# Optimization experiments

Hardware: AMD Instinct MI355X
Metric: run time of the kernel (lower is better)

Reference implementation:

```python
import jax, jax.numpy as jnp
import numpy as np
from jax.ops import segment_sum

NEG_SLOPE = 0.01  # torch F.leaky_relu default

N_NODES = 100000
N_EDGES = 1600000
IN_FEAT = 67
HIDDEN = 256
N_CLASS = 18
N_GRAPHS = 256


def setup_inputs() -> dict:
    key = jax.random.key(0)
    ks = jax.random.split(key, 12)
    h = jax.random.normal(ks[0], (N_NODES, IN_FEAT), dtype=jnp.float32)
    src = jax.random.randint(ks[1], (N_EDGES,), 0, N_NODES, dtype=jnp.int32)
    dst = jax.random.randint(ks[2], (N_EDGES,), 0, N_NODES, dtype=jnp.int32)
    graph_ids = jnp.sort(jax.random.randint(ks[3], (N_NODES,), 0, N_GRAPHS, dtype=jnp.int32))
    s = 0.05
    W1_self = jax.random.normal(ks[4], (IN_FEAT, HIDDEN), dtype=jnp.float32) * s
    W1_neigh = jax.random.normal(ks[5], (IN_FEAT, HIDDEN), dtype=jnp.float32) * s
    b1 = jnp.zeros((HIDDEN,), dtype=jnp.float32)
    W2_self = jax.random.normal(ks[6], (HIDDEN, HIDDEN), dtype=jnp.float32) * s
    W2_neigh = jax.random.normal(ks[7], (HIDDEN, HIDDEN), dtype=jnp.float32) * s
    b2 = jnp.zeros((HIDDEN,), dtype=jnp.float32)
    Wfc = jax.random.normal(ks[8], (HIDDEN, N_CLASS), dtype=jnp.float32) * s
    bfc = jnp.zeros((N_CLASS,), dtype=jnp.float32)
    return {
        "h": h, "W1_self": W1_self, "W1_neigh": W1_neigh, "b1": b1,
        "W2_self": W2_self, "W2_neigh": W2_neigh, "b2": b2,
        "Wfc": Wfc, "bfc": bfc,
        "src": src, "dst": dst, "graph_ids": graph_ids, "num_graphs": N_GRAPHS,
    }


def _sage_mean(h, Wself, Wneigh, b, src, dst, n_nodes):
    # DGL SAGEConv(mean): h_neigh = mean over incoming neighbors; 0 if no neighbors
    agg = segment_sum(h[src], dst, num_segments=n_nodes)          # [N, D]
    deg = segment_sum(jnp.ones_like(dst, dtype=h.dtype), dst, num_segments=n_nodes)
    h_neigh = agg / jnp.maximum(deg, 1.0)[:, None]
    return h @ Wself + h_neigh @ Wneigh + b


def reference(h, W1_self, W1_neigh, b1, W2_self, W2_neigh, b2, Wfc, bfc,
              src, dst, graph_ids, num_graphs):
    n_nodes = h.shape[0]
    x = jax.nn.leaky_relu(_sage_mean(h, W1_self, W1_neigh, b1, src, dst, n_nodes), NEG_SLOPE)
    x = jax.nn.leaky_relu(_sage_mean(x, W2_self, W2_neigh, b2, src, dst, n_nodes), NEG_SLOPE)
    # dgl.mean_nodes: per-graph mean pooling over nodes
    gsum = segment_sum(x, graph_ids, num_segments=num_graphs)       # [G, D]
    gcnt = segment_sum(jnp.ones((n_nodes,), dtype=x.dtype), graph_ids, num_segments=num_graphs)
    hg = gsum / jnp.maximum(gcnt, 1.0)[:, None]
    return hg @ Wfc + bfc  # [G, n_classifier]
```

## Files before the change

kernel.cpp:

```cpp
#include <hip/hip_runtime.h>

#define WAVE 64
#define OW 256
#define LDA1 96

typedef short bf16x8 __attribute__((ext_vector_type(8)));
typedef float f32x4  __attribute__((ext_vector_type(4)));

__device__ __forceinline__ unsigned short f2bf(float f) {
    unsigned int u = __float_as_uint(f);
    u = (u + 0x7FFF + ((u >> 16) & 1)) >> 16;
    return (unsigned short)u;
}
__device__ __forceinline__ float bf2f(unsigned short u) {
    return __uint_as_float(((unsigned int)u) << 16);
}
__device__ __forceinline__ float bflo(unsigned int u) { return __uint_as_float(u << 16); }
__device__ __forceinline__ float bfhi(unsigned int u) { return __uint_as_float(u & 0xFFFF0000u); }
__device__ __forceinline__ unsigned int packbf(float lo, float hi) {
    return (unsigned int)f2bf(lo) | ((unsigned int)f2bf(hi) << 16);
}
__device__ __forceinline__ float lrelu(float x) { return x > 0.0f ? x : 0.01f * x; }


__device__ __forceinline__ void pack_b_body(const float* __restrict__ Ws,
                                            const float* __restrict__ Wn,
                                            unsigned short* __restrict__ Bb,
                                            int KHALF, int KT_HALF, int idx) {
    int e  = idx & 7;
    int l  = (idx >> 3) & 63;
    int nt = (idx >> 9) & 15;
    int kt = idx >> 13;
    int n  = nt * 16 + (l & 15);
    int kh = (kt < KT_HALF ? kt : kt - KT_HALF) * 32 + (l >> 4) * 8 + e;
    const float* W = (kt < KT_HALF) ? Ws : Wn;
    float v = (kh < KHALF) ? W[(size_t)kh * OW + n] : 0.0f;
    Bb[idx] = f2bf(v);
}

__global__ void prep_kernel(const float* __restrict__ h, unsigned int* __restrict__ hb,
                            int N, int K,
                            const float* __restrict__ W1s, const float* __restrict__ W1n,
                            unsigned short* __restrict__ Bb1,
                            const float* __restrict__ W2s, const float* __restrict__ W2n,
                            unsigned short* __restrict__ Bb2,
                            const int* __restrict__ dst, int* __restrict__ cnt,
                            int* __restrict__ rank, int E) {
    const int tid = blockIdx.x * blockDim.x + threadIdx.x;
    const int nth = gridDim.x * blockDim.x;

    const int tot_h = N * (LDA1 / 2);
    for (int i = tid; i < tot_h; i += nth) {
        int row = i / (LDA1 / 2);
        int c   = (i - row * (LDA1 / 2)) * 2;
        float v0 = (c     < K) ? h[(size_t)row * K + c]     : 0.0f;
        float v1 = (c + 1 < K) ? h[(size_t)row * K + c + 1] : 0.0f;
        hb[i] = packbf(v0, v1);
    }
    for (int i = tid; i < 2 * 3 * 16 * 64 * 8; i += nth)
        pack_b_body(W1s, W1n, Bb1, K, 3, i);
    for (int i = tid; i < 2 * 8 * 16 * 64 * 8; i += nth)
        pack_b_body(W2s, W2n, Bb2, OW, 8, i);
    const int e4 = E >> 2;
    const int4* dst4 = (const int4*)dst;
    int4* rank4 = (int4*)rank;
    for (int i = tid; i < e4; i += nth) {
        int4 d = dst4[i];
        int4 r;
        r.x = atomicAdd(&cnt[d.x], 1);
        r.y = atomicAdd(&cnt[d.y], 1);
        r.z = atomicAdd(&cnt[d.z], 1);
        r.w = atomicAdd(&cnt[d.w], 1);
        rank4[i] = r;
    }
    for (int e = e4 * 4 + tid; e < E; e += nth)
        rank[e] = atomicAdd(&cnt[dst[e]], 1);
}


__global__ __launch_bounds__(1024) void scan_blocksum(const int* __restrict__ cnt,
                                                      int* __restrict__ bsum, int n) {
    __shared__ int s[1024];
    int i = blockIdx.x * 1024 + threadIdx.x;
    s[threadIdx.x] = (i < n) ? cnt[i] : 0;
    __syncthreads();
    for (int off = 512; off > 0; off >>= 1) {
        if (threadIdx.x < off) s[threadIdx.x] += s[threadIdx.x + off];
        __syncthreads();
    }
    if (threadIdx.x == 0) bsum[blockIdx.x] = s[0];
}

__global__ __launch_bounds__(128) void scan_offsets(int* __restrict__ bsum, int nb) {
    __shared__ int s[128];
    int v = (threadIdx.x < nb) ? bsum[threadIdx.x] : 0;
    s[threadIdx.x] = v;
    __syncthreads();
    for (int off = 1; off < 128; off <<= 1) {
        int t = (threadIdx.x >= off) ? s[threadIdx.x - off] : 0;
        __syncthreads();
        s[threadIdx.x] += t;
        __syncthreads();
    }
    if (threadIdx.x < nb) bsum[threadIdx.x] = s[threadIdx.x] - v;
}

__global__ __launch_bounds__(1024) void scan_write(const int* __restrict__ cnt,
                                                   const int* __restrict__ boff,
                                                   int* __restrict__ rowptr, int n) {
    __shared__ int s[1024];
    int i = blockIdx.x * 1024 + threadIdx.x;
    int v = (i < n) ? cnt[i] : 0;
    s[threadIdx.x] = v;
    __syncthreads();
    for (int off = 1; off < 1024; off <<= 1) {
        int t = (threadIdx.x >= off) ? s[threadIdx.x - off] : 0;
        __syncthreads();
        s[threadIdx.x] += t;
        __syncthreads();
    }
    if (i < n) rowptr[i + 1] = boff[blockIdx.x] + s[threadIdx.x];
    if (i == 0) rowptr[0] = 0;
}

__global__ void fill_kernel(const int* __restrict__ src, const int* __restrict__ dst,
                            const int* __restrict__ rank, const int* __restrict__ rowptr,
                            int* __restrict__ csr_src, int E) {
    const int tid = blockIdx.x * blockDim.x + threadIdx.x;
    const int nth = gridDim.x * blockDim.x;
    const int e4 = E >> 2;
    const int4* dst4 = (const int4*)dst;
    const int4* src4 = (const int4*)src;
    const int4* rank4 = (const int4*)rank;
    for (int i = tid; i < e4; i += nth) {
        int4 d = dst4[i];
        int4 s = src4[i];
        int4 r = rank4[i];
        csr_src[rowptr[d.x] + r.x] = s.x;
        csr_src[rowptr[d.y] + r.y] = s.y;
        csr_src[rowptr[d.z] + r.z] = s.z;
        csr_src[rowptr[d.w] + r.w] = s.w;
    }
    for (int e = e4 * 4 + tid; e < E; e += nth)
        csr_src[rowptr[dst[e]] + rank[e]] = src[e];
}


__global__ void gather_mean256_half(const unsigned int* __restrict__ feat,
                                    const int* __restrict__ rowptr, const int* __restrict__ csr,
                                    unsigned int* __restrict__ aggm, int N, int colhalf) {
    const int lane = threadIdx.x & (WAVE - 1);
    const int grp  = lane >> 4;
    const int sub  = lane & 15;
    const int cb   = colhalf * 64;
    int wave = (blockIdx.x * blockDim.x + threadIdx.x) / WAVE;
    int nw   = (gridDim.x * blockDim.x) / WAVE;

    for (int v = wave; v < N; v += nw) {
        const int beg = rowptr[v], deg = rowptr[v + 1] - beg;
        float l0 = 0.f, h0 = 0.f, l1 = 0.f, h1 = 0.f,
              l2 = 0.f, h2 = 0.f, l3 = 0.f, h3 = 0.f;

        const int noct = deg >> 3;
        for (int i = 0; i < noct; ++i) {
            int e0 = csr[beg + 8 * i + grp];
            int e1 = csr[beg + 8 * i + 4 + grp];
            uint4 x0 = *(const uint4*)(feat + (size_t)e0 * 128 + cb + sub * 4);
            uint4 x1 = *(const uint4*)(feat + (size_t)e1 * 128 + cb + sub * 4);
            l0 += bflo(x0.x) + bflo(x1.x); h0 += bfhi(x0.x) + bfhi(x1.x);
            l1 += bflo(x0.y) + bflo(x1.y); h1 += bfhi(x0.y) + bfhi(x1.y);
            l2 += bflo(x0.z) + bflo(x1.z); h2 += bfhi(x0.z) + bfhi(x1.z);
            l3 += bflo(x0.w) + bflo(x1.w); h3 += bfhi(x0.w) + bfhi(x1.w);
        }
        for (int e = (noct << 3) + grp; e < deg; e += 4) {
            int s = csr[beg + e];
            uint4 x = *(const uint4*)(feat + (size_t)s * 128 + cb + sub * 4);
            l0 += bflo(x.x); h0 += bfhi(x.x);
            l1 += bflo(x.y); h1 += bfhi(x.y);
            l2 += bflo(x.z); h2 += bfhi(x.z);
            l3 += bflo(x.w); h3 += bfhi(x.w);
        }
        l0 += __shfl_xor(l0, 16); l0 += __shfl_xor(l0, 32);
        h0 += __shfl_xor(h0, 16); h0 += __shfl_xor(h0, 32);
        l1 += __shfl_xor(l1, 16); l1 += __shfl_xor(l1, 32);
        h1 += __shfl_xor(h1, 16); h1 += __shfl_xor(h1, 32);
        l2 += __shfl_xor(l2, 16); l2 += __shfl_xor(l2, 32);
        h2 += __shfl_xor(h2, 16); h2 += __shfl_xor(h2, 32);
        l3 += __shfl_xor(l3, 16); l3 += __shfl_xor(l3, 32);
        h3 += __shfl_xor(h3, 16); h3 += __shfl_xor(h3, 32);

        if (grp == 0) {
            float inv = 1.0f / fmaxf((float)deg, 1.0f);
            uint4 o;
            o.x = packbf(l0 * inv, h0 * inv);
            o.y = packbf(l1 * inv, h1 * inv);
            o.z = packbf(l2 * inv, h2 * inv);
            o.w = packbf(l3 * inv, h3 * inv);
            *(uint4*)(aggm + (size_t)v * 128 + cb + sub * 4) = o;
        }
    }
}

__global__ void gather_mean_pad(const unsigned int* __restrict__ feat,
                                const int* __restrict__ rowptr, const int* __restrict__ csr,
                                unsigned int* __restrict__ aggm, int N) {
    const int lane = threadIdx.x & (WAVE - 1);
    const int half = lane >> 5;
    const int sub  = lane & 31;
    const bool act = sub < 24;
    int wave = (blockIdx.x * blockDim.x + threadIdx.x) / WAVE;
    int nw   = (gridDim.x * blockDim.x) / WAVE;

    for (int v = wave; v < N; v += nw) {
        const int beg = rowptr[v], deg = rowptr[v + 1] - beg;
        const int npairs = deg >> 1;
        float l0 = 0.f, h0 = 0.f, l1 = 0.f, h1 = 0.f;

        int p = 0;
        for (; p + 3 < npairs; p += 4) {
            int i0 = csr[beg + 2 * (p + 0) + half];
            int i1 = csr[beg + 2 * (p + 1) + half];
            int i2 = csr[beg + 2 * (p + 2) + half];
            int i3 = csr[beg + 2 * (p + 3) + half];
            if (act) {
                uint2 x0 = *(const uint2*)(feat + (size_t)i0 * 48 + sub * 2);
                uint2 x1 = *(const uint2*)(feat + (size_t)i1 * 48 + sub * 2);
                uint2 x2 = *(const uint2*)(feat + (size_t)i2 * 48 + sub * 2);
                uint2 x3 = *(const uint2*)(feat + (size_t)i3 * 48 + sub * 2);
                l0 += bflo(x0.x) + bflo(x1.x) + bflo(x2.x) + bflo(x3.x);
                h0 += bfhi(x0.x) + bfhi(x1.x) + bfhi(x2.x) + bfhi(x3.x);
                l1 += bflo(x0.y) + bflo(x1.y) + bflo(x2.y) + bflo(x3.y);
                h1 += bfhi(x0.y) + bfhi(x1.y) + bfhi(x2.y) + bfhi(x3.y);
            }
        }
        for (; p < npairs; ++p) {
            int i0 = csr[beg + 2 * p + half];
            if (act) {
                uint2 x0 = *(const uint2*)(feat + (size_t)i0 * 48 + sub * 2);
                l0 += bflo(x0.x); h0 += bfhi(x0.x);
                l1 += bflo(x0.y); h1 += bfhi(x0.y);
            }
        }
        if ((deg & 1) && half == 0) {
            int i0 = csr[beg + deg - 1];
            if (act) {
                uint2 x0 = *(const uint2*)(feat + (size_t)i0 * 48 + sub * 2);
                l0 += bflo(x0.x); h0 += bfhi(x0.x);
                l1 += bflo(x0.y); h1 += bfhi(x0.y);
            }
        }
        l0 += __shfl_xor(l0, 32); h0 += __shfl_xor(h0, 32);
        l1 += __shfl_xor(l1, 32); h1 += __shfl_xor(h1, 32);

        if (half == 0 && act) {
            float inv = 1.0f / fmaxf((float)deg, 1.0f);
            uint2 o;
            o.x = packbf(l0 * inv, h0 * inv);
            o.y = packbf(l1 * inv, h1 * inv);
            *(uint2*)(aggm + (size_t)v * 48 + sub * 2) = o;
        }
    }
}

template<int KT_HALF, int CHUNK>
__global__ __launch_bounds__(512) void sage_mfma(
    const unsigned short* __restrict__ Hs, const unsigned short* __restrict__ Hn, int lda,
    const unsigned short* __restrict__ Bb, const float* __restrict__ bias,
    unsigned short* __restrict__ outb, int M)
{
    constexpr int NT    = 2 * KT_HALF;
    constexpr int NCH   = NT / CHUNK;
    constexpr int CELEM = CHUNK * 16 * 64;
    constexpr int CPT   = CELEM / 512;
    __shared__ bf16x8 Bs[CELEM];

    const int t    = threadIdx.x;
    const int lane = t & 63, wid = t >> 6;
    const int wm   = wid >> 1, wn = wid & 1;
    const int brow = blockIdx.x * 128;
    const int lrow = lane & 15, kblk = lane >> 4;

    const int r0 = brow + wm * 32 + lrow;
    const int r1 = r0 + 16;
    const int r0c = (r0 < M) ? r0 : (M - 1);
    const int r1c = (r1 < M) ? r1 : (M - 1);

    f32x4 acc[2][8];
#pragma unroll
    for (int rt = 0; rt < 2; ++rt)
#pragma unroll
        for (int ct = 0; ct < 8; ++ct) acc[rt][ct] = (f32x4)0.0f;

    for (int ch = 0; ch < NCH; ++ch) {
        bf16x8 a0[CHUNK], a1[CHUNK];
#pragma unroll
        for (int k = 0; k < CHUNK; ++k) {
            int kt = ch * CHUNK + k;
            bool self = kt < KT_HALF;
            int kh = (self ? kt : kt - KT_HALF) * 32 + kblk * 8;
            const unsigned short* srcp = self ? Hs : Hn;
            a0[k] = *(const bf16x8*)(srcp + (size_t)r0c * lda + kh);
            a1[k] = *(const bf16x8*)(srcp + (size_t)r1c * lda + kh);
        }
        const bf16x8* gB = (const bf16x8*)Bb + (size_t)ch * CELEM;
        bf16x8 tmp[CPT];
#pragma unroll
        for (int i = 0; i < CPT; ++i) tmp[i] = gB[i * 512 + t];
        __syncthreads();
#pragma unroll
        for (int i = 0; i < CPT; ++i) Bs[i * 512 + t] = tmp[i];
        __syncthreads();
#pragma unroll
        for (int k = 0; k < CHUNK; ++k) {
            const bf16x8* bp = &Bs[(k * 16 + wn * 8) * 64 + lane];
#pragma unroll
            for (int ct = 0; ct < 8; ++ct) {
                bf16x8 b = bp[ct * 64];
                acc[0][ct] = __builtin_amdgcn_mfma_f32_16x16x32_bf16(a0[k], b, acc[0][ct], 0, 0, 0);
                acc[1][ct] = __builtin_amdgcn_mfma_f32_16x16x32_bf16(a1[k], b, acc[1][ct], 0, 0, 0);
            }
        }
    }

#pragma unroll
    for (int rt = 0; rt < 2; ++rt) {
        int rbase = brow + wm * 32 + rt * 16 + kblk * 4;
#pragma unroll
        for (int ct = 0; ct < 8; ++ct) {
            int col = wn * 128 + ct * 16 + lrow;
            float vb = bias[col];
#pragma unroll
            for (int j = 0; j < 4; ++j) {
                int row = rbase + j;
                if (row < M)
                    outb[(size_t)row * OW + col] = f2bf(lrelu(acc[rt][ct][j] + vb));
            }
        }
    }
}


__global__ __launch_bounds__(256) void pool_fc_kernel(
    const unsigned short* __restrict__ x, const int* __restrict__ gid,
    const float* __restrict__ Wfc, const float* __restrict__ bfc,
    float* __restrict__ out, int N, int C)
{
    int g = blockIdx.x;
    int lo = 0, hi = N;
    while (lo < hi) { int m = (lo + hi) >> 1; if (gid[m] < g) lo = m + 1; else hi = m; }
    int beg = lo;
    hi = N;
    while (lo < hi) { int m = (lo + hi) >> 1; if (gid[m] <= g) lo = m + 1; else hi = m; }
    int end = lo;

    __shared__ float hg[OW];
    int c = threadIdx.x;
    float s0 = 0.f, s1 = 0.f, s2 = 0.f, s3 = 0.f;
    int r = beg;
    for (; r + 3 < end; r += 4) {
        s0 += bf2f(x[(size_t)(r + 0) * OW + c]);
        s1 += bf2f(x[(size_t)(r + 1) * OW + c]);
        s2 += bf2f(x[(size_t)(r + 2) * OW + c]);
        s3 += bf2f(x[(size_t)(r + 3) * OW + c]);
    }
    for (; r < end; ++r) s0 += bf2f(x[(size_t)r * OW + c]);
    float s = (s0 + s1) + (s2 + s3);
    float inv = (end > beg) ? 1.0f / (float)(end - beg) : 0.0f;
    hg[c] = s * inv;
    __syncthreads();

    if (c < C) {
        float a = bfc[c];
        for (int k = 0; k < OW; ++k)
            a = fmaf(hg[k], Wfc[(size_t)k * C + c], a);
        out[(size_t)g * C + c] = a;
    }
}

extern "C" void kernel_launch(void* const* d_in, const int* in_sizes, int n_in,
                              void* d_out, int out_size, void* d_ws, size_t ws_size,
                              hipStream_t stream) {
    const float* h   = (const float*)d_in[0];
    const float* W1s = (const float*)d_in[1];
    const float* W1n = (const float*)d_in[2];
    const float* b1  = (const float*)d_in[3];
    const float* W2s = (const float*)d_in[4];
    const float* W2n = (const float*)d_in[5];
    const float* b2  = (const float*)d_in[6];
    const float* Wfc = (const float*)d_in[7];
    const float* bfc = (const float*)d_in[8];
    const int*   src = (const int*)d_in[9];
    const int*   dst = (const int*)d_in[10];
    const int*   gid = (const int*)d_in[11];

    const int N  = in_sizes[11];
    const int E  = in_sizes[9];
    const int K1 = in_sizes[0] / N;
    const int NC = in_sizes[8];
    const int G  = out_size / NC;

    char* w = (char*)d_ws;
    auto alloc = [&](size_t bytes) { char* p = w; w += (bytes + 255) & ~(size_t)255; return p; };
    unsigned int*   hb     = (unsigned int*)alloc((size_t)N * (LDA1 / 2) * 4);
    unsigned int*   agg1b  = (unsigned int*)alloc((size_t)N * (LDA1 / 2) * 4);
    unsigned short* x1b    = (unsigned short*)alloc((size_t)N * OW * 2);
    unsigned short* agg2b  = (unsigned short*)alloc((size_t)N * OW * 2);
    int*            rowptr = (int*)alloc((size_t)(N + 1) * 4);
    int*            cnt    = (int*)alloc((size_t)N * 4);
    int*            csr    = (int*)alloc((size_t)E * 4);
    int*            rank   = (int*)alloc((size_t)E * 4);
    int*            bsum   = (int*)alloc(1024 * 4);
    unsigned short* Bb1    = (unsigned short*)alloc((size_t)2 * 3 * 16 * 64 * 8 * 2);
    unsigned short* Bb2    = (unsigned short*)alloc((size_t)2 * 8 * 16 * 64 * 8 * 2);

    float* out = (float*)d_out;
    const int nb = (N + 1023) / 1024;

    hipMemsetAsync(cnt, 0, (size_t)N * sizeof(int), stream);
    prep_kernel<<<2048, 256, 0, stream>>>(h, hb, N, K1, W1s, W1n, Bb1, W2s, W2n, Bb2,
                                          dst, cnt, rank, E);

    scan_blocksum<<<nb, 1024, 0, stream>>>(cnt, bsum, N);
    scan_offsets<<<1, 128, 0, stream>>>(bsum, nb);
    scan_write<<<nb, 1024, 0, stream>>>(cnt, bsum, rowptr, N);
    fill_kernel<<<2048, 256, 0, stream>>>(src, dst, rank, rowptr, csr, E);

    const int gemm_grid = (N + 127) / 128;

    gather_mean_pad<<<4096, 256, 0, stream>>>(hb, rowptr, csr, agg1b, N);
    sage_mfma<3, 3><<<gemm_grid, 512, 0, stream>>>((const unsigned short*)hb,
                                                   (const unsigned short*)agg1b, LDA1,
                                                   Bb1, b1, x1b, N);

    gather_mean256_half<<<4096, 256, 0, stream>>>((const unsigned int*)x1b, rowptr, csr,
                                                  (unsigned int*)agg2b, N, 0);
    gather_mean256_half<<<4096, 256, 0, stream>>>((const unsigned int*)x1b, rowptr, csr,
                                                  (unsigned int*)agg2b, N, 1);
    sage_mfma<8, 4><<<gemm_grid, 512, 0, stream>>>(x1b, agg2b, OW, Bb2, b2, x1b, N);

    pool_fc_kernel<<<G, 256, 0, stream>>>(x1b, gid, Wfc, bfc, out, N, NC);
}
```

Before: 441.9 us.

## Build CSR via chunked LDS histograms instead of global atomic counting

Replaces the global-atomic degree count and rank assignment with a two-level scheme. Each block builds a shared-memory histogram with packed 16-bit counters over one edge chunk and one node partition, then a per-node scan across chunks gives the offsets, and the fill step combines rowptr, the chunk offset and the local rank. This is meant to remove contended global atomics on cnt and to halve rank storage. In exchange it reads dst once per partition (4x), writes and reads a 64xN histogram (~25MB), and adds a kernel launch.

```diff
diff --git a/kernel.cpp b/kernel.cpp
--- a/kernel.cpp
+++ b/kernel.cpp
@@ -3,6 +3,10 @@
 #define WAVE 64
 #define OW 256
 #define LDA1 96
+#define NCHUNK 64
+#define PBITS 15
+#define PBINS (1 << PBITS)
+#define NPART 4
 
 typedef short bf16x8 __attribute__((ext_vector_type(8)));
 typedef float f32x4  __attribute__((ext_vector_type(4)));
@@ -43,9 +47,7 @@
                             const float* __restrict__ W1s, const float* __restrict__ W1n,
                             unsigned short* __restrict__ Bb1,
                             const float* __restrict__ W2s, const float* __restrict__ W2n,
-                            unsigned short* __restrict__ Bb2,
-                            const int* __restrict__ dst, int* __restrict__ cnt,
-                            int* __restrict__ rank, int E) {
+                            unsigned short* __restrict__ Bb2) {
     const int tid = blockIdx.x * blockDim.x + threadIdx.x;
     const int nth = gridDim.x * blockDim.x;
 
@@ -61,22 +63,55 @@
         pack_b_body(W1s, W1n, Bb1, K, 3, i);
     for (int i = tid; i < 2 * 8 * 16 * 64 * 8; i += nth)
         pack_b_body(W2s, W2n, Bb2, OW, 8, i);
-    const int e4 = E >> 2;
-    const int4* dst4 = (const int4*)dst;
-    int4* rank4 = (int4*)rank;
-    for (int i = tid; i < e4; i += nth) {
-        int4 d = dst4[i];
-        int4 r;
-        r.x = atomicAdd(&cnt[d.x], 1);
-        r.y = atomicAdd(&cnt[d.y], 1);
-        r.z = atomicAdd(&cnt[d.z], 1);
-        r.w = atomicAdd(&cnt[d.w], 1);
-        rank4[i] = r;
-    }
-    for (int e = e4 * 4 + tid; e < E; e += nth)
-        rank[e] = atomicAdd(&cnt[dst[e]], 1);
-}
-
+}
+
+
+__global__ __launch_bounds__(512) void hist_kernel(const int* __restrict__ dst, int E, int N,
+                                                   int* __restrict__ hist,
+                                                   unsigned short* __restrict__ rank_local) {
+    __shared__ unsigned int lcnt[PBINS / 2];
+    const int c    = blockIdx.x / NPART;
+    const int p    = blockIdx.x - c * NPART;
+    const int base = p << PBITS;
+    const int nb   = (N - base < PBINS) ? (N - base) : PBINS;
+    if (nb <= 0) return;
+    const int che = (E + NCHUNK - 1) / NCHUNK;
+    const int beg = c * che;
+    const int end = (beg + che < E) ? (beg + che) : E;
+
+    for (int i = threadIdx.x; i < PBINS / 2; i += 512) lcnt[i] = 0;
+    __syncthreads();
+
+    for (int e = beg + (int)threadIdx.x; e < end; e += 512) {
+        int d = dst[e] - base;
+        if ((unsigned)d < (unsigned)nb) {
+            unsigned int sh  = (d & 1) * 16;
+            unsigned int old = atomicAdd(&lcnt[d >> 1], 1u << sh);
+            rank_local[e] = (unsigned short)((old >> sh) & 0xFFFFu);
+        }
+    }
+    __syncthreads();
+
+    int* hrow = hist + (size_t)c * N + base;
+    for (int i = threadIdx.x; i < nb; i += 512) {
+        unsigned int v = lcnt[i >> 1];
+        hrow[i] = (int)((v >> ((i & 1) * 16)) & 0xFFFFu);
+    }
+}
+
+__global__ void chunk_scan_kernel(int* __restrict__ hist, int* __restrict__ cnt, int N) {
+    int bin = blockIdx.x * blockDim.x + threadIdx.x;
+    if (bin >= N) return;
+    int s = 0;
+#pragma unroll 8
+    for (int c = 0; c < NCHUNK; ++c) {
+        size_t idx = (size_t)c * N + bin;
+        int t = hist[idx];
+        hist[idx] = s;
+        s += t;
+    }
+    cnt[bin] = s;
+}
 
 __global__ __launch_bounds__(1024) void scan_blocksum(const int* __restrict__ cnt,
                                                       int* __restrict__ bsum, int n) {
@@ -124,25 +159,18 @@
 }
 
 __global__ void fill_kernel(const int* __restrict__ src, const int* __restrict__ dst,
-                            const int* __restrict__ rank, const int* __restrict__ rowptr,
-                            int* __restrict__ csr_src, int E) {
+                            const unsigned short* __restrict__ rank_local,
+                            const int* __restrict__ rowptr, const int* __restrict__ hist,
+                            int* __restrict__ csr, int E, int N) {
+    const int che = (E + NCHUNK - 1) / NCHUNK;
     const int tid = blockIdx.x * blockDim.x + threadIdx.x;
     const int nth = gridDim.x * blockDim.x;
-    const int e4 = E >> 2;
-    const int4* dst4 = (const int4*)dst;
-    const int4* src4 = (const int4*)src;
-    const int4* rank4 = (const int4*)rank;
-    for (int i = tid; i < e4; i += nth) {
-        int4 d = dst4[i];
-        int4 s = src4[i];
-        int4 r = rank4[i];
-        csr_src[rowptr[d.x] + r.x] = s.x;
-        csr_src[rowptr[d.y] + r.y] = s.y;
-        csr_src[rowptr[d.z] + r.z] = s.z;
-        csr_src[rowptr[d.w] + r.w] = s.w;
-    }
-    for (int e = e4 * 4 + tid; e < E; e += nth)
-        csr_src[rowptr[dst[e]] + rank[e]] = src[e];
+    for (int e = tid; e < E; e += nth) {
+        int d = dst[e];
+        int c = e / che;
+        int pos = rowptr[d] + hist[(size_t)c * N + d] + (int)rank_local[e];
+        csr[pos] = src[e];
+    }
 }
 
 
@@ -408,7 +436,8 @@
     int*            rowptr = (int*)alloc((size_t)(N + 1) * 4);
     int*            cnt    = (int*)alloc((size_t)N * 4);
     int*            csr    = (int*)alloc((size_t)E * 4);
-    int*            rank   = (int*)alloc((size_t)E * 4);
+    unsigned short* rankl  = (unsigned short*)alloc((size_t)E * 2);
+    int*            hist   = (int*)alloc((size_t)NCHUNK * N * 4);
     int*            bsum   = (int*)alloc(1024 * 4);
     unsigned short* Bb1    = (unsigned short*)alloc((size_t)2 * 3 * 16 * 64 * 8 * 2);
     unsigned short* Bb2    = (unsigned short*)alloc((size_t)2 * 8 * 16 * 64 * 8 * 2);
@@ -416,14 +445,14 @@
     float* out = (float*)d_out;
     const int nb = (N + 1023) / 1024;
 
-    hipMemsetAsync(cnt, 0, (size_t)N * sizeof(int), stream);
-    prep_kernel<<<2048, 256, 0, stream>>>(h, hb, N, K1, W1s, W1n, Bb1, W2s, W2n, Bb2,
-                                          dst, cnt, rank, E);
-
+    hist_kernel<<<NCHUNK * NPART, 512, 0, stream>>>(dst, E, N, hist, rankl);
+    chunk_scan_kernel<<<(N + 255) / 256, 256, 0, stream>>>(hist, cnt, N);
     scan_blocksum<<<nb, 1024, 0, stream>>>(cnt, bsum, N);
     scan_offsets<<<1, 128, 0, stream>>>(bsum, nb);
     scan_write<<<nb, 1024, 0, stream>>>(cnt, bsum, rowptr, N);
-    fill_kernel<<<2048, 256, 0, stream>>>(src, dst, rank, rowptr, csr, E);
+    fill_kernel<<<2048, 256, 0, stream>>>(src, dst, rankl, rowptr, hist, csr, E, N);
+
+    prep_kernel<<<2048, 256, 0, stream>>>(h, hb, N, K1, W1s, W1n, Bb1, W2s, W2n, Bb2);
 
     const int gemm_grid = (N + 127) / 128;
 
```

Measured after the change: 426.5 us. -3.5%, faster.
